# Optimization experiments

Measured on AMD Instinct MI355X. Metric: run time of the kernel, lower is better.

## Reference

```python
import jax, jax.numpy as jnp
import numpy as np
from jax import lax

B, N, M, K, C_IN = 4, 8192, 2048, 64, 64
RADIUS = 0.2
OUT_DIMS = [64, 64, 128]
BN_EPS = 1e-5


def _fps(pts):
    # pts: (N,3) -> (M,) int32 furthest-point-sampling indices, seeded at index 0
    n = pts.shape[0]
    def step(carry, _):
        mind, last = carry
        d = jnp.sum((pts - pts[last]) ** 2, axis=-1)   # dist^2 to newest centroid
        mind = jnp.minimum(mind, d)                    # dist^2 to selected set
        nxt = jnp.argmax(mind).astype(jnp.int32)
        return (mind, nxt), nxt
    init = (jnp.full((n,), 1e10, pts.dtype), jnp.int32(0))
    _, rest = lax.scan(step, init, None, length=M - 1)
    return jnp.concatenate([jnp.zeros((1,), jnp.int32), rest])


def _ball_query(qp, sp):
    # qp: (M,3) centroids, sp: (N,3) -> (M,K) first K in-radius indices, padded with first hit
    d2 = jnp.sum((qp[:, None, :] - sp[None, :, :]) ** 2, axis=-1)  # (M,N)
    score = jnp.where(d2 < RADIUS ** 2, jnp.arange(N, dtype=jnp.int32), jnp.int32(N))
    idx = -lax.top_k(-score, K)[0]          # K smallest scores = first K in-radius indices
    valid = idx < N
    first = jnp.where(valid[:, :1], idx[:, :1], 0)  # pointnet2 pads with first neighbor (or 0)
    return jnp.where(valid, idx, first)


def _forward(s_points, s_feats, Ws, gs, bs):
    pts = jnp.transpose(s_points, (0, 2, 1))    # (B,N,3)
    feats = jnp.transpose(s_feats, (0, 2, 1))   # (B,N,C)
    fps_idx = jax.vmap(_fps)(pts)               # (B,M)
    q = jnp.take_along_axis(pts, fps_idx[:, :, None], axis=1)      # (B,M,3)
    nbr_idx = jax.vmap(_ball_query)(q, pts)     # (B,M,K)
    nbr_pts = jax.vmap(lambda p, i: p[i])(pts, nbr_idx)            # (B,M,K,3)
    nbr_fts = jax.vmap(lambda f, i: f[i])(feats, nbr_idx)          # (B,M,K,C)
    # mini-PointNet input: [relative coords, neighbor feats] -> (B,M,K,3+C)
    x = jnp.concatenate([nbr_pts - q[:, :, None, :], nbr_fts], axis=-1)
    for W, g, b in zip(Ws, gs, bs):
        x = jnp.einsum('bmkc,oc->bmko', x, W)   # shared 1x1 conv
        mu = jnp.mean(x, axis=(0, 1, 2), keepdims=True)             # BatchNorm (train-mode stats)
        var = jnp.mean((x - mu) ** 2, axis=(0, 1, 2), keepdims=True)
        x = jax.nn.relu((x - mu) * lax.rsqrt(var + BN_EPS) * g + b)
    q_feats = jnp.transpose(jnp.max(x, axis=2), (0, 2, 1))          # max-pool over K -> (B,C_out,M)
    return jnp.transpose(q, (0, 2, 1)), q_feats


def setup_inputs() -> dict:
    key = jax.random.key(0)
    ks = jax.random.split(key, 8)
    inp = {
        's_points': jax.random.uniform(ks[0], (B, 3, N), jnp.float32),
        's_feats': jax.random.normal(ks[1], (B, C_IN, N), jnp.float32),
    }
    dims = [C_IN + 3] + OUT_DIMS
    for i in range(3):
        inp[f'W{i}'] = jax.random.normal(ks[2 + i], (dims[i + 1], dims[i]), jnp.float32) / np.float32(np.sqrt(dims[i]))
        inp[f'g{i}'] = jnp.ones((dims[i + 1],), jnp.float32)
        inp[f'b{i}'] = jnp.zeros((dims[i + 1],), jnp.float32)
    return inp


def reference(s_points, s_feats, W0, g0, b0, W1, g1, b1, W2, g2, b2):
    return _forward(s_points, s_feats, (W0, W1, W2), (g0, g1, g2), (b0, b1, b2))
```

## Files before the change

kernel.cpp:

```cpp
#include <hip/hip_runtime.h>
#include <math.h>


constexpr int B = 4, N = 8192, M = 2048, K = 64;
constexpr int C0 = 67;
constexpr int NB_CHAIN = B * M;
constexpr int NROW = B * M * K;

#define DEVFN static __device__ __forceinline__

template <int CTRL>
DEVFN float dpp_shift0(float x) {
  return __uint_as_float((unsigned)__builtin_amdgcn_update_dpp(
      0, (int)__float_as_uint(x), CTRL, 0xf, 0xf, true));
}

__global__ __launch_bounds__(256) void transpose_kernel(
    const float* __restrict__ P, const float* __restrict__ F,
    float4* __restrict__ pts4, float* __restrict__ ft)
{
  int g = blockIdx.x * 256 + threadIdx.x;
  int b = g >> 13, i = g & (N - 1);
  const float* Pb = P + (size_t)b * 3 * N;
  pts4[g] = make_float4(Pb[i], Pb[N + i], Pb[2 * N + i], 0.f);
  const float* Fb = F + (size_t)b * 64 * N;
  float* o = ft + (size_t)g * 64;
  #pragma unroll 8
  for (int c = 0; c < 64; ++c) o[c] = Fb[(size_t)c * N + i];
}

__global__ __launch_bounds__(256) void prep_weights(
    const float* __restrict__ W0, const float* __restrict__ W1,
    const float* __restrict__ W2,
    float* __restrict__ w0T, float* __restrict__ w1T, float* __restrict__ w2T)
{
  int t = threadIdx.x;
  for (int x = t; x < 67 * 64; x += 256) { int k = x >> 6, o = x & 63;  w0T[x] = W0[o * 67 + k]; }
  for (int x = t; x < 64 * 64; x += 256) { int k = x >> 6, o = x & 63;  w1T[x] = W1[o * 64 + k]; }
  for (int x = t; x < 64 * 128; x += 256){ int k = x >> 7, o = x & 127; w2T[x] = W2[o * 64 + k]; }
}

constexpr int FPS_T = 512;
constexpr int FPS_PT = N / FPS_T;

__global__ __launch_bounds__(512) void fps_kernel(
    const float* __restrict__ P, float4* __restrict__ q4, float* __restrict__ out_q)
{
  __shared__ float4 sp4[N];
  __shared__ __align__(16) unsigned long long partial[2][8];
  __shared__ unsigned short swidx[M];
  const int b = blockIdx.x, tid = threadIdx.x;
  const float* Pb = P + (size_t)b * 3 * N;

  float px[FPS_PT], py[FPS_PT], pz[FPS_PT], mind[FPS_PT];
  #pragma unroll
  for (int j = 0; j < FPS_PT; ++j) {
    int i = tid * FPS_PT + j;
    px[j] = Pb[i]; py[j] = Pb[N + i]; pz[j] = Pb[2 * N + i];
    sp4[i] = make_float4(px[j], py[j], pz[j], 0.f);
    mind[j] = 1e10f;
  }
  if (tid == 0) swidx[0] = 0;
  __syncthreads();

  float cx = Pb[0], cy = Pb[N], cz = Pb[2 * N];

  for (int s = 1; s < M; ++s) {
    float bv = -1.f; int bi = 0;
    #pragma unroll
    for (int j = 0; j < FPS_PT; ++j) {
      float dx = __fsub_rn(px[j], cx), dy = __fsub_rn(py[j], cy), dz = __fsub_rn(pz[j], cz);
      float d  = __fadd_rn(__fadd_rn(__fmul_rn(dx, dx), __fmul_rn(dy, dy)), __fmul_rn(dz, dz));
      float mm = fminf(mind[j], d);
      mind[j] = mm;
      bool tk = mm > bv;
      bv = tk ? mm : bv;
      bi = tk ? tid * FPS_PT + j : bi;
    }
    float r = bv;
    r = fmaxf(r, dpp_shift0<0x111>(r));
    r = fmaxf(r, dpp_shift0<0x112>(r));
    r = fmaxf(r, dpp_shift0<0x114>(r));
    r = fmaxf(r, dpp_shift0<0x118>(r));
    r = fmaxf(r, dpp_shift0<0x142>(r));
    r = fmaxf(r, dpp_shift0<0x143>(r));
    float wv = __shfl(r, 63);
    unsigned long long tied = __ballot(bv == wv);
    int wl = __ffsll(tied) - 1;
    int wi = __shfl(bi, wl);
    unsigned long long key =
        ((unsigned long long)__float_as_uint(wv) << 32) | (unsigned int)(~wi);
    const int buf = s & 1;
    if ((tid & 63) == 0) partial[buf][tid >> 6] = key;
    __syncthreads();
    unsigned long long k0 = partial[buf][0];
    #pragma unroll
    for (int w = 1; w < 8; ++w) {
      unsigned long long o = partial[buf][w];
      k0 = (o > k0) ? o : k0;
    }
    const int widx = (int)(~(unsigned int)(k0 & 0xFFFFFFFFull));
    const float4 c = sp4[widx];
    cx = c.x; cy = c.y; cz = c.z;
    if (tid == 0) swidx[s] = (unsigned short)widx;
  }
  __syncthreads();
  for (int s = tid; s < M; s += FPS_T) {
    const float4 c = sp4[swidx[s]];
    q4[b * M + s] = c;
    out_q[b * 3 * M + s]         = c.x;
    out_q[b * 3 * M + M + s]     = c.y;
    out_q[b * 3 * M + 2 * M + s] = c.z;
  }
}

__global__ __launch_bounds__(256) void ballquery_kernel(
    const float4* __restrict__ pts4, const float4* __restrict__ q4, int* __restrict__ nbr)
{
  __shared__ int slot[4][K];
  const int wv = threadIdx.x >> 6, lane = threadIdx.x & 63;
  const int qid = blockIdx.x * 4 + wv;
  const int b = qid >> 11;
  const float4 qc = q4[qid];
  const float4* pb = pts4 + (size_t)b * N;
  const float r2 = 0.04f;
  int count = 0;
  for (int c0 = 0; c0 < N; c0 += 64) {
    float4 p = pb[c0 + lane];
    float dx = __fsub_rn(p.x, qc.x), dy = __fsub_rn(p.y, qc.y), dz = __fsub_rn(p.z, qc.z);
    float d2 = __fadd_rn(__fadd_rn(__fmul_rn(dx, dx), __fmul_rn(dy, dy)), __fmul_rn(dz, dz));
    bool in = d2 < r2;
    unsigned long long mask = __ballot(in);
    int pos = count + (int)__popcll(mask & ((1ull << lane) - 1ull));
    if (in && pos < K) slot[wv][pos] = c0 + lane;
    count += (int)__popcll(mask);
    if (count >= K) break;
  }
  __syncthreads();
  int valid = count < K ? count : K;
  int v = 0;
  if (valid > 0) {
    int first = slot[wv][0];
    v = (lane < valid) ? slot[wv][lane] : first;
  }
  nbr[(size_t)qid * K + lane] = v;
}

DEVFN void conv_tile(float acc[8][8], const float (&xt)[C0 + 1][64],
                     const float* __restrict__ wT, int KK, int OC, int choff, int rg)
{
  #pragma unroll
  for (int i = 0; i < 8; ++i)
    #pragma unroll
    for (int j = 0; j < 8; ++j) acc[i][j] = 0.f;
  for (int k = 0; k < KK; ++k) {
    const float4 xa = *(const float4*)&xt[k][rg * 8];
    const float4 xb = *(const float4*)&xt[k][rg * 8 + 4];
    const float4 wa = *(const float4*)(wT + (size_t)k * OC + choff);
    const float4 wb = *(const float4*)(wT + (size_t)k * OC + choff + 4);
    const float xs[8] = {xa.x, xa.y, xa.z, xa.w, xb.x, xb.y, xb.z, xb.w};
    const float wv[8] = {wa.x, wa.y, wa.z, wa.w, wb.x, wb.y, wb.z, wb.w};
    #pragma unroll
    for (int i = 0; i < 8; ++i)
      #pragma unroll
      for (int j = 0; j < 8; ++j) acc[i][j] = fmaf(xs[i], wv[j], acc[i][j]);
  }
}

DEVFN void bn_relu_store(const float acc[8][8], const float* __restrict__ sc,
                         const float* __restrict__ sh, int choff, int rg,
                         float (&xt)[C0 + 1][64])
{
  float4 s0 = *(const float4*)(sc + choff), s1 = *(const float4*)(sc + choff + 4);
  float4 h0 = *(const float4*)(sh + choff), h1 = *(const float4*)(sh + choff + 4);
  const float scv[8] = {s0.x, s0.y, s0.z, s0.w, s1.x, s1.y, s1.z, s1.w};
  const float shv[8] = {h0.x, h0.y, h0.z, h0.w, h1.x, h1.y, h1.z, h1.w};
  __syncthreads();
  #pragma unroll
  for (int j = 0; j < 8; ++j) {
    float4 a, b;
    a.x = fmaxf(fmaf(acc[0][j], scv[j], shv[j]), 0.f);
    a.y = fmaxf(fmaf(acc[1][j], scv[j], shv[j]), 0.f);
    a.z = fmaxf(fmaf(acc[2][j], scv[j], shv[j]), 0.f);
    a.w = fmaxf(fmaf(acc[3][j], scv[j], shv[j]), 0.f);
    b.x = fmaxf(fmaf(acc[4][j], scv[j], shv[j]), 0.f);
    b.y = fmaxf(fmaf(acc[5][j], scv[j], shv[j]), 0.f);
    b.z = fmaxf(fmaf(acc[6][j], scv[j], shv[j]), 0.f);
    b.w = fmaxf(fmaf(acc[7][j], scv[j], shv[j]), 0.f);
    *(float4*)&xt[choff + j][rg * 8]     = a;
    *(float4*)&xt[choff + j][rg * 8 + 4] = b;
  }
  __syncthreads();
}

DEVFN void stats_tile(const float acc[8][8], int chbase, int lane, int qid,
                      float* __restrict__ Psum, float* __restrict__ Psq)
{
  #pragma unroll
  for (int j = 0; j < 8; ++j) {
    float s = 0.f, q = 0.f;
    #pragma unroll
    for (int i = 0; i < 8; ++i) { s += acc[i][j]; q = fmaf(acc[i][j], acc[i][j], q); }
    s += __shfl_xor(s, 8);  q += __shfl_xor(q, 8);
    s += __shfl_xor(s, 16); q += __shfl_xor(q, 16);
    s += __shfl_xor(s, 32); q += __shfl_xor(q, 32);
    if ((lane >> 3) == 0) {
      Psum[(size_t)(chbase + j) * NB_CHAIN + qid] = s;
      Psq [(size_t)(chbase + j) * NB_CHAIN + qid] = q;
    }
  }
}

DEVFN void maxmin_tile(const float acc[8][8], int chbase, int lane, int qid,
                       float* __restrict__ ymax, float* __restrict__ ymin)
{
  #pragma unroll
  for (int j = 0; j < 8; ++j) {
    float mx = acc[0][j], mn = acc[0][j];
    #pragma unroll
    for (int i = 1; i < 8; ++i) { mx = fmaxf(mx, acc[i][j]); mn = fminf(mn, acc[i][j]); }
    mx = fmaxf(mx, __shfl_xor(mx, 8));  mn = fminf(mn, __shfl_xor(mn, 8));
    mx = fmaxf(mx, __shfl_xor(mx, 16)); mn = fminf(mn, __shfl_xor(mn, 16));
    mx = fmaxf(mx, __shfl_xor(mx, 32)); mn = fminf(mn, __shfl_xor(mn, 32));
    if ((lane >> 3) == 0) {
      ymax[(size_t)(chbase + j) * NB_CHAIN + qid] = mx;
      ymin[(size_t)(chbase + j) * NB_CHAIN + qid] = mn;
    }
  }
}

DEVFN void gather_x0(const float4* __restrict__ pts4, const float* __restrict__ ft,
                     const float4* __restrict__ q4, const int* __restrict__ nbr,
                     int qid, int b, int lane, float (&xt)[C0 + 1][64])
{
  const int i = nbr[(size_t)qid * K + lane];
  const float4 qc = q4[qid];
  const float4 p = pts4[(size_t)b * N + i];
  xt[0][lane] = p.x - qc.x;
  xt[1][lane] = p.y - qc.y;
  xt[2][lane] = p.z - qc.z;
  const float4* fr = (const float4*)(ft + (size_t)(b * N + i) * 64);
  #pragma unroll
  for (int c = 0; c < 16; ++c) {
    float4 f = fr[c];
    xt[3 + 4 * c + 0][lane] = f.x;
    xt[3 + 4 * c + 1][lane] = f.y;
    xt[3 + 4 * c + 2][lane] = f.z;
    xt[3 + 4 * c + 3][lane] = f.w;
  }
  __syncthreads();
}

DEVFN void y_store(const float acc[8][8], float* __restrict__ y, int qid, int rg, int cg)
{
  float* base = y + (size_t)qid * 4096 + (size_t)(cg * 8) * 64 + rg * 8;
  #pragma unroll
  for (int j = 0; j < 8; ++j) {
    float4 a = make_float4(acc[0][j], acc[1][j], acc[2][j], acc[3][j]);
    float4 c = make_float4(acc[4][j], acc[5][j], acc[6][j], acc[7][j]);
    *(float4*)(base + (size_t)j * 64)     = a;
    *(float4*)(base + (size_t)j * 64 + 4) = c;
  }
}
DEVFN void y_load(float acc[8][8], const float* __restrict__ y, int qid, int rg, int cg)
{
  const float* base = y + (size_t)qid * 4096 + (size_t)(cg * 8) * 64 + rg * 8;
  #pragma unroll
  for (int j = 0; j < 8; ++j) {
    float4 a = *(const float4*)(base + (size_t)j * 64);
    float4 c = *(const float4*)(base + (size_t)j * 64 + 4);
    acc[0][j] = a.x; acc[1][j] = a.y; acc[2][j] = a.z; acc[3][j] = a.w;
    acc[4][j] = c.x; acc[5][j] = c.y; acc[6][j] = c.z; acc[7][j] = c.w;
  }
}

__global__ __launch_bounds__(64) void chain_p1(
    const float4* __restrict__ pts4, const float* __restrict__ ft,
    const float4* __restrict__ q4, const int* __restrict__ nbr,
    const float* __restrict__ w0T,
    float* __restrict__ Psum, float* __restrict__ Psq, float* __restrict__ y)
{
  __shared__ float xt[C0 + 1][64];
  const int qid = blockIdx.x, b = qid >> 11, lane = threadIdx.x;
  const int rg = lane >> 3, cg = lane & 7;
  gather_x0(pts4, ft, q4, nbr, qid, b, lane, xt);
  float acc[8][8];
  conv_tile(acc, xt, w0T, 67, 64, cg * 8, rg);
  stats_tile(acc, cg * 8, lane, qid, Psum, Psq);
  y_store(acc, y, qid, rg, cg);
}

template <int LAYER>
__global__ __launch_bounds__(64) void chain_p23(
    const float* __restrict__ wT, const float* __restrict__ sc,
    const float* __restrict__ sh,
    float* __restrict__ Psum, float* __restrict__ Psq,
    float* __restrict__ y, float* __restrict__ ymax, float* __restrict__ ymin)
{
  __shared__ float xt[C0 + 1][64];
  const int qid = blockIdx.x, lane = threadIdx.x;
  const int rg = lane >> 3, cg = lane & 7;
  float acc[8][8];
  y_load(acc, y, qid, rg, cg);
  bn_relu_store(acc, sc, sh, cg * 8, rg, xt);
  if (LAYER == 2) {
    conv_tile(acc, xt, wT, 64, 64, cg * 8, rg);
    stats_tile(acc, cg * 8, lane, qid, Psum, Psq);
    y_store(acc, y, qid, rg, cg);
  } else {
    conv_tile(acc, xt, wT, 64, 128, cg * 8, rg);
    stats_tile(acc, cg * 8, lane, qid, Psum, Psq);
    maxmin_tile(acc, cg * 8, lane, qid, ymax, ymin);
    conv_tile(acc, xt, wT, 64, 128, 64 + cg * 8, rg);
    stats_tile(acc, 64 + cg * 8, lane, qid, Psum, Psq);
    maxmin_tile(acc, 64 + cg * 8, lane, qid, ymax, ymin);
  }
}

template <int PHASE>
__global__ __launch_bounds__(64) void chain_kernel(
    const float4* __restrict__ pts4, const float* __restrict__ ft,
    const float4* __restrict__ q4, const int* __restrict__ nbr,
    const float* __restrict__ w0T, const float* __restrict__ w1T, const float* __restrict__ w2T,
    const float* __restrict__ sc1, const float* __restrict__ sh1,
    const float* __restrict__ sc2, const float* __restrict__ sh2,
    float* __restrict__ Psum, float* __restrict__ Psq,
    float* __restrict__ ymax, float* __restrict__ ymin)
{
  __shared__ float xt[C0 + 1][64];
  const int qid = blockIdx.x, b = qid >> 11, lane = threadIdx.x;
  const int rg = lane >> 3, cg = lane & 7;
  gather_x0(pts4, ft, q4, nbr, qid, b, lane, xt);
  float acc[8][8];
  conv_tile(acc, xt, w0T, 67, 64, cg * 8, rg);
  if (PHASE == 1) { stats_tile(acc, cg * 8, lane, qid, Psum, Psq); return; }
  bn_relu_store(acc, sc1, sh1, cg * 8, rg, xt);
  conv_tile(acc, xt, w1T, 64, 64, cg * 8, rg);
  if (PHASE == 2) { stats_tile(acc, cg * 8, lane, qid, Psum, Psq); return; }
  bn_relu_store(acc, sc2, sh2, cg * 8, rg, xt);
  conv_tile(acc, xt, w2T, 64, 128, cg * 8, rg);
  stats_tile(acc, cg * 8, lane, qid, Psum, Psq);
  maxmin_tile(acc, cg * 8, lane, qid, ymax, ymin);
  conv_tile(acc, xt, w2T, 64, 128, 64 + cg * 8, rg);
  stats_tile(acc, 64 + cg * 8, lane, qid, Psum, Psq);
  maxmin_tile(acc, 64 + cg * 8, lane, qid, ymax, ymin);
}

__global__ __launch_bounds__(256) void reduce_stats(
    const float* __restrict__ Psum, const float* __restrict__ Psq,
    const float* __restrict__ g, const float* __restrict__ beta,
    float* __restrict__ scale, float* __restrict__ shift)
{
  __shared__ float ls[256], lq[256];
  const int o = blockIdx.x, t = threadIdx.x;
  float s = 0.f, q = 0.f;
  for (int x = t; x < NB_CHAIN; x += 256) {
    s += Psum[(size_t)o * NB_CHAIN + x];
    q += Psq [(size_t)o * NB_CHAIN + x];
  }
  ls[t] = s; lq[t] = q;
  __syncthreads();
  for (int st = 128; st > 0; st >>= 1) {
    if (t < st) { ls[t] += ls[t + st]; lq[t] += lq[t + st]; }
    __syncthreads();
  }
  if (t == 0) {
    const float inv = 1.f / (float)NROW;
    float mu = ls[0] * inv;
    float var = lq[0] * inv - mu * mu;
    float scv = g[o] / sqrtf(var + 1e-5f);
    scale[o] = scv;
    shift[o] = beta[o] - mu * scv;
  }
}

__global__ __launch_bounds__(256) void bn_final(
    const float* __restrict__ ymax, const float* __restrict__ ymin,
    const float* __restrict__ sc3, const float* __restrict__ sh3,
    float* __restrict__ out1)
{
  const int idx = blockIdx.x * 256 + threadIdx.x;
  const int ch = (idx >> 11) & 127;
  const int qid = ((idx >> 18) << 11) | (idx & 2047);
  const float sc = sc3[ch], sh = sh3[ch];
  const float v = (sc >= 0.f) ? ymax[(size_t)ch * NB_CHAIN + qid]
                              : ymin[(size_t)ch * NB_CHAIN + qid];
  out1[idx] = fmaxf(fmaf(v, sc, sh), 0.f);
}

extern "C" void kernel_launch(void* const* d_in, const int* in_sizes, int n_in,
                              void* d_out, int out_size, void* d_ws, size_t ws_size,
                              hipStream_t stream)
{
  const float* P  = (const float*)d_in[0];
  const float* F  = (const float*)d_in[1];
  const float* W0 = (const float*)d_in[2];
  const float* g0 = (const float*)d_in[3];
  const float* b0 = (const float*)d_in[4];
  const float* W1 = (const float*)d_in[5];
  const float* g1 = (const float*)d_in[6];
  const float* b1 = (const float*)d_in[7];
  const float* W2 = (const float*)d_in[8];
  const float* g2 = (const float*)d_in[9];
  const float* b2 = (const float*)d_in[10];

  float* out_q = (float*)d_out;
  float* out_f = out_q + B * 3 * M;

  char* w = (char*)d_ws;
  size_t off = 0;
  auto alloc = [&](size_t bytes) -> void* {
    off = (off + 255) & ~(size_t)255;
    void* p = w + off;
    off += bytes;
    return p;
  };
  float4* pts4 = (float4*)alloc((size_t)B * N * sizeof(float4));
  float*  ft   = (float*) alloc((size_t)B * N * 64 * 4);
  float*  w0T  = (float*) alloc(68 * 64 * 4);
  float*  w1T  = (float*) alloc(64 * 64 * 4);
  float*  w2T  = (float*) alloc(64 * 128 * 4);
  float4* q4   = (float4*)alloc((size_t)B * M * sizeof(float4));
  int*    nbr  = (int*)   alloc((size_t)B * M * K * 4);
  float*  Psum = (float*) alloc((size_t)128 * NB_CHAIN * 4);
  float*  Psq  = (float*) alloc((size_t)128 * NB_CHAIN * 4);
  float*  ymax = (float*) alloc((size_t)128 * NB_CHAIN * 4);
  float*  ymin = (float*) alloc((size_t)128 * NB_CHAIN * 4);
  float*  bnp  = (float*) alloc(6 * 128 * 4);
  float *sc1 = bnp, *sh1 = bnp + 128, *sc2 = bnp + 256, *sh2 = bnp + 384,
        *sc3 = bnp + 512, *sh3 = bnp + 640;
  const size_t ybytes = (size_t)NB_CHAIN * 64 * 64 * 4;
  off = (off + 255) & ~(size_t)255;
  const bool have_y = (off + ybytes) <= ws_size;
  float* y = (float*)(w + off);
  (void)in_sizes; (void)n_in; (void)out_size;

  transpose_kernel<<<B * N / 256, 256, 0, stream>>>(P, F, pts4, ft);
  prep_weights<<<1, 256, 0, stream>>>(W0, W1, W2, w0T, w1T, w2T);
  fps_kernel<<<B, FPS_T, 0, stream>>>(P, q4, out_q);
  ballquery_kernel<<<B * M / 4, 256, 0, stream>>>(pts4, q4, nbr);

  if (have_y) {
    chain_p1<<<NB_CHAIN, 64, 0, stream>>>(pts4, ft, q4, nbr, w0T, Psum, Psq, y);
    reduce_stats<<<64, 256, 0, stream>>>(Psum, Psq, g0, b0, sc1, sh1);
    chain_p23<2><<<NB_CHAIN, 64, 0, stream>>>(w1T, sc1, sh1, Psum, Psq, y, ymax, ymin);
    reduce_stats<<<64, 256, 0, stream>>>(Psum, Psq, g1, b1, sc2, sh2);
    chain_p23<3><<<NB_CHAIN, 64, 0, stream>>>(w2T, sc2, sh2, Psum, Psq, y, ymax, ymin);
    reduce_stats<<<128, 256, 0, stream>>>(Psum, Psq, g2, b2, sc3, sh3);
  } else {
    chain_kernel<1><<<NB_CHAIN, 64, 0, stream>>>(pts4, ft, q4, nbr, w0T, w1T, w2T,
        sc1, sh1, sc2, sh2, Psum, Psq, ymax, ymin);
    reduce_stats<<<64, 256, 0, stream>>>(Psum, Psq, g0, b0, sc1, sh1);
    chain_kernel<2><<<NB_CHAIN, 64, 0, stream>>>(pts4, ft, q4, nbr, w0T, w1T, w2T,
        sc1, sh1, sc2, sh2, Psum, Psq, ymax, ymin);
    reduce_stats<<<64, 256, 0, stream>>>(Psum, Psq, g1, b1, sc2, sh2);
    chain_kernel<3><<<NB_CHAIN, 64, 0, stream>>>(pts4, ft, q4, nbr, w0T, w1T, w2T,
        sc1, sh1, sc2, sh2, Psum, Psq, ymax, ymin);
    reduce_stats<<<128, 256, 0, stream>>>(Psum, Psq, g2, b2, sc3, sh3);
  }
  bn_final<<<NB_CHAIN * 128 / 256, 256, 0, stream>>>(ymax, ymin, sc3, sh3, out_f);
}
```

Before: 2.346 ms.

## Prune FPS work with spatial cell bounding boxes and per-cell max keys

Rewrites furthest-point sampling to bin points into 128 spatial cells sorted in shared memory, each with a bounding box and a cached best (mindist, index) key. Each iteration updates only the cells whose bounding box lies closer to the new centroid than their current max min-distance, then reduces the 128 cell keys. This avoids touching all 8192 points every step. In exchange it adds extra syncs per iteration, lower parallelism when few cells are active, and more complex tie-breaking logic.

```diff
diff --git a/kernel.cpp b/kernel.cpp
--- a/kernel.cpp
+++ b/kernel.cpp
@@ -13,6 +13,29 @@
 DEVFN float dpp_shift0(float x) {
   return __uint_as_float((unsigned)__builtin_amdgcn_update_dpp(
       0, (int)__float_as_uint(x), CTRL, 0xf, 0xf, true));
+}
+template <int CTRL>
+DEVFN unsigned dpp_shift0u(unsigned x) {
+  return (unsigned)__builtin_amdgcn_update_dpp(0, (int)x, CTRL, 0xf, 0xf, true);
+}
+DEVFN float wave_max_f32(float x) {
+  x = fmaxf(x, dpp_shift0<0x111>(x));
+  x = fmaxf(x, dpp_shift0<0x112>(x));
+  x = fmaxf(x, dpp_shift0<0x114>(x));
+  x = fmaxf(x, dpp_shift0<0x118>(x));
+  x = fmaxf(x, dpp_shift0<0x142>(x));
+  x = fmaxf(x, dpp_shift0<0x143>(x));
+  return __shfl(x, 63);
+}
+DEVFN unsigned wave_max_u32(unsigned x) {
+  unsigned t;
+  t = dpp_shift0u<0x111>(x); x = x > t ? x : t;
+  t = dpp_shift0u<0x112>(x); x = x > t ? x : t;
+  t = dpp_shift0u<0x114>(x); x = x > t ? x : t;
+  t = dpp_shift0u<0x118>(x); x = x > t ? x : t;
+  t = dpp_shift0u<0x142>(x); x = x > t ? x : t;
+  t = dpp_shift0u<0x143>(x); x = x > t ? x : t;
+  return (unsigned)__shfl((int)x, 63);
 }
 
 __global__ __launch_bounds__(256) void transpose_kernel(
@@ -41,76 +64,154 @@
 }
 
 constexpr int FPS_T = 512;
-constexpr int FPS_PT = N / FPS_T;
 
 __global__ __launch_bounds__(512) void fps_kernel(
     const float* __restrict__ P, float4* __restrict__ q4, float* __restrict__ out_q)
 {
-  __shared__ float4 sp4[N];
-  __shared__ __align__(16) unsigned long long partial[2][8];
+  __shared__ float sx[N], sy[N], sz[N];
+  __shared__ float smind[N];
+  __shared__ unsigned short ssidx[N];
+  __shared__ float bb[6][128];
+  __shared__ unsigned long long bkey[128];
+  __shared__ unsigned short bspos[128];
+  __shared__ int starts[129];
+  __shared__ int hist[128];
+  __shared__ unsigned short act[2][64];
+  __shared__ int nact[2];
   __shared__ unsigned short swidx[M];
+  __shared__ float cc[3];
+  __shared__ int spos0;
+
   const int b = blockIdx.x, tid = threadIdx.x;
+  const int wv = tid >> 6, lane = tid & 63;
   const float* Pb = P + (size_t)b * 3 * N;
 
-  float px[FPS_PT], py[FPS_PT], pz[FPS_PT], mind[FPS_PT];
-  #pragma unroll
-  for (int j = 0; j < FPS_PT; ++j) {
-    int i = tid * FPS_PT + j;
-    px[j] = Pb[i]; py[j] = Pb[N + i]; pz[j] = Pb[2 * N + i];
-    sp4[i] = make_float4(px[j], py[j], pz[j], 0.f);
-    mind[j] = 1e10f;
-  }
-  if (tid == 0) swidx[0] = 0;
-  __syncthreads();
-
-  float cx = Pb[0], cy = Pb[N], cz = Pb[2 * N];
+  float lx[16], ly[16], lz[16]; int lcid[16];
+  if (tid < 128) hist[tid] = 0;
+  __syncthreads();
+  #pragma unroll
+  for (int j = 0; j < 16; ++j) {
+    int i = tid + j * FPS_T;
+    lx[j] = Pb[i]; ly[j] = Pb[N + i]; lz[j] = Pb[2 * N + i];
+    int cxi = min((int)(lx[j] * 4.f), 3);
+    int cyi = min((int)(ly[j] * 4.f), 3);
+    int czi = min((int)(lz[j] * 8.f), 7);
+    lcid[j] = (cxi << 5) | (cyi << 3) | czi;
+    atomicAdd(&hist[lcid[j]], 1);
+  }
+  __syncthreads();
+  if (tid == 0) {
+    int acc = 0;
+    for (int k = 0; k < 128; ++k) { starts[k] = acc; acc += hist[k]; }
+    starts[128] = acc;
+  }
+  __syncthreads();
+  if (tid < 128) hist[tid] = starts[tid];
+  __syncthreads();
+  #pragma unroll
+  for (int j = 0; j < 16; ++j) {
+    int i = tid + j * FPS_T;
+    int pos = atomicAdd(&hist[lcid[j]], 1);
+    sx[pos] = lx[j]; sy[pos] = ly[j]; sz[pos] = lz[j];
+    ssidx[pos] = (unsigned short)i;
+    smind[pos] = 1e10f;
+    if (i == 0) spos0 = pos;
+  }
+  __syncthreads();
+  if (tid < 128) {
+    int s0 = starts[tid], s1 = starts[tid + 1];
+    float xlo = 1e30f, xhi = -1e30f, ylo = 1e30f, yhi = -1e30f, zlo = 1e30f, zhi = -1e30f;
+    unsigned mor = 0; unsigned short msp = 0;
+    for (int p = s0; p < s1; ++p) {
+      float x = sx[p], y = sy[p], z = sz[p];
+      xlo = fminf(xlo, x); xhi = fmaxf(xhi, x);
+      ylo = fminf(ylo, y); yhi = fmaxf(yhi, y);
+      zlo = fminf(zlo, z); zhi = fmaxf(zhi, z);
+      unsigned no = ~(unsigned)ssidx[p];
+      if (no > mor) { mor = no; msp = (unsigned short)p; }
+    }
+    bb[0][tid] = xlo; bb[1][tid] = xhi; bb[2][tid] = ylo;
+    bb[3][tid] = yhi; bb[4][tid] = zlo; bb[5][tid] = zhi;
+    bkey[tid] = (s1 > s0)
+        ? (((unsigned long long)__float_as_uint(1e10f) << 32) | mor) : 0ull;
+    bspos[tid] = msp;
+  }
+  if (tid == 0) swidx[0] = (unsigned short)spos0;
+  __syncthreads();
+  float cx = sx[spos0], cy = sy[spos0], cz = sz[spos0];
 
   for (int s = 1; s < M; ++s) {
-    float bv = -1.f; int bi = 0;
-    #pragma unroll
-    for (int j = 0; j < FPS_PT; ++j) {
-      float dx = __fsub_rn(px[j], cx), dy = __fsub_rn(py[j], cy), dz = __fsub_rn(pz[j], cz);
-      float d  = __fadd_rn(__fadd_rn(__fmul_rn(dx, dx), __fmul_rn(dy, dy)), __fmul_rn(dz, dz));
-      float mm = fminf(mind[j], d);
-      mind[j] = mm;
-      bool tk = mm > bv;
-      bv = tk ? mm : bv;
-      bi = tk ? tid * FPS_PT + j : bi;
+    if (tid < 128) {
+      float ax = fmaxf(0.f, fmaxf(__fsub_rn(bb[0][tid], cx), __fsub_rn(cx, bb[1][tid])));
+      float ay = fmaxf(0.f, fmaxf(__fsub_rn(bb[2][tid], cy), __fsub_rn(cy, bb[3][tid])));
+      float az = fmaxf(0.f, fmaxf(__fsub_rn(bb[4][tid], cz), __fsub_rn(cz, bb[5][tid])));
+      float dlow = __fadd_rn(__fadd_rn(__fmul_rn(ax, ax), __fmul_rn(ay, ay)), __fmul_rn(az, az));
+      float ub = __uint_as_float((unsigned)(bkey[tid] >> 32));
+      bool actv = dlow < ub;
+      unsigned long long am = __ballot(actv);
+      int pos = (int)__popcll(am & ((1ull << lane) - 1ull));
+      if (actv) act[wv][pos] = (unsigned short)tid;
+      if (lane == 0) nact[wv] = (int)__popcll(am);
     }
-    float r = bv;
-    r = fmaxf(r, dpp_shift0<0x111>(r));
-    r = fmaxf(r, dpp_shift0<0x112>(r));
-    r = fmaxf(r, dpp_shift0<0x114>(r));
-    r = fmaxf(r, dpp_shift0<0x118>(r));
-    r = fmaxf(r, dpp_shift0<0x142>(r));
-    r = fmaxf(r, dpp_shift0<0x143>(r));
-    float wv = __shfl(r, 63);
-    unsigned long long tied = __ballot(bv == wv);
-    int wl = __ffsll(tied) - 1;
-    int wi = __shfl(bi, wl);
-    unsigned long long key =
-        ((unsigned long long)__float_as_uint(wv) << 32) | (unsigned int)(~wi);
-    const int buf = s & 1;
-    if ((tid & 63) == 0) partial[buf][tid >> 6] = key;
     __syncthreads();
-    unsigned long long k0 = partial[buf][0];
-    #pragma unroll
-    for (int w = 1; w < 8; ++w) {
-      unsigned long long o = partial[buf][w];
-      k0 = (o > k0) ? o : k0;
+    const int n0 = nact[0], ntot = n0 + nact[1];
+    for (int a = wv; a < ntot; a += 8) {
+      int k = (a < n0) ? act[0][a] : act[1][a - n0];
+      int s0 = starts[k], s1 = starts[k + 1];
+      unsigned long long bestk = 0ull, myrec = 0ull;
+      int cp = 0;
+      for (int off = s0; off < s1; off += 64) {
+        int p = off + lane;
+        float nm = -1.f; unsigned mor = 0u;
+        if (p < s1) {
+          float dx = __fsub_rn(sx[p], cx), dy = __fsub_rn(sy[p], cy), dz = __fsub_rn(sz[p], cz);
+          float d = __fadd_rn(__fadd_rn(__fmul_rn(dx, dx), __fmul_rn(dy, dy)), __fmul_rn(dz, dz));
+          nm = fminf(smind[p], d);
+          smind[p] = nm;
+          mor = ~(unsigned)ssidx[p];
+        }
+        float wvmax = wave_max_f32(nm);
+        unsigned cand = (nm == wvmax) ? mor : 0u;
+        unsigned wor = wave_max_u32(cand);
+        unsigned long long kk =
+            ((unsigned long long)__float_as_uint(wvmax) << 32) | wor;
+        if (nm == wvmax && mor == wor && kk > myrec) { myrec = kk; cp = p; }
+        if (kk > bestk) bestk = kk;
+      }
+      if (myrec == bestk && bestk != 0ull) {
+        bkey[k] = bestk;
+        bspos[k] = (unsigned short)cp;
+      }
     }
-    const int widx = (int)(~(unsigned int)(k0 & 0xFFFFFFFFull));
-    const float4 c = sp4[widx];
-    cx = c.x; cy = c.y; cz = c.z;
-    if (tid == 0) swidx[s] = (unsigned short)widx;
-  }
-  __syncthreads();
-  for (int s = tid; s < M; s += FPS_T) {
-    const float4 c = sp4[swidx[s]];
-    q4[b * M + s] = c;
-    out_q[b * 3 * M + s]         = c.x;
-    out_q[b * 3 * M + M + s]     = c.y;
-    out_q[b * 3 * M + 2 * M + s] = c.z;
+    __syncthreads();
+    if (wv == 0) {
+      unsigned long long k1 = bkey[lane], k2 = bkey[lane + 64];
+      unsigned long long kk = k1 > k2 ? k1 : k2;
+      float vh = __uint_as_float((unsigned)(kk >> 32));
+      float vmax = wave_max_f32(vh);
+      unsigned cand = (vh == vmax) ? (unsigned)(kk & 0xFFFFFFFFull) : 0u;
+      unsigned lomax = wave_max_u32(cand);
+      unsigned long long fin =
+          ((unsigned long long)__float_as_uint(vmax) << 32) | lomax;
+      int kwin = -1;
+      if (k1 == fin) kwin = lane;
+      if (k2 == fin) kwin = lane + 64;
+      if (kwin >= 0) {
+        int sp = bspos[kwin];
+        cc[0] = sx[sp]; cc[1] = sy[sp]; cc[2] = sz[sp];
+        swidx[s] = (unsigned short)sp;
+      }
+    }
+    __syncthreads();
+    cx = cc[0]; cy = cc[1]; cz = cc[2];
+  }
+  for (int s2 = tid; s2 < M; s2 += FPS_T) {
+    int sp = swidx[s2];
+    float xx = sx[sp], yy = sy[sp], zz = sz[sp];
+    q4[b * M + s2] = make_float4(xx, yy, zz, 0.f);
+    out_q[b * 3 * M + s2]         = xx;
+    out_q[b * 3 * M + M + s2]     = yy;
+    out_q[b * 3 * M + 2 * M + s2] = zz;
   }
 }
 
```

Result: slower. 3.417 ms (+45.6%).

## Spatially sort FPS points into voxel buckets and skip threads via bounding-box pruning

Applied to the files above, without the earlier changes.

The FPS kernel now buckets points into an 8x8x8 voxel grid with a shared-memory counting sort, so each thread holds 16 spatially clustered points and tracks their bounding box. Each iteration, a wave skips the distance update when no lane's box can come closer to the new centroid than that lane's current best min-distance, since the min-distance values cannot change in that case. Tie-breaking now carries the original index through the comparison, and the wave reduction uses DPP plus readlane in place of a shuffle and ballot. This adds sort setup and per-iteration box checks, and it only saves work when whole waves can be skipped.

```diff
diff --git a/kernel.cpp b/kernel.cpp
--- a/kernel.cpp
+++ b/kernel.cpp
@@ -13,6 +13,30 @@
 DEVFN float dpp_shift0(float x) {
   return __uint_as_float((unsigned)__builtin_amdgcn_update_dpp(
       0, (int)__float_as_uint(x), CTRL, 0xf, 0xf, true));
+}
+template <int CTRL>
+DEVFN unsigned dpp_shift0u(unsigned x) {
+  return (unsigned)__builtin_amdgcn_update_dpp(0, (int)x, CTRL, 0xf, 0xf, true);
+}
+DEVFN float wave_max_bcast_f(float x) {
+  x = fmaxf(x, dpp_shift0<0x111>(x));
+  x = fmaxf(x, dpp_shift0<0x112>(x));
+  x = fmaxf(x, dpp_shift0<0x114>(x));
+  x = fmaxf(x, dpp_shift0<0x118>(x));
+  x = fmaxf(x, dpp_shift0<0x142>(x));
+  x = fmaxf(x, dpp_shift0<0x143>(x));
+  return __uint_as_float(
+      (unsigned)__builtin_amdgcn_readlane((int)__float_as_uint(x), 63));
+}
+DEVFN unsigned wave_max_bcast_u(unsigned x) {
+  unsigned t;
+  t = dpp_shift0u<0x111>(x); x = x > t ? x : t;
+  t = dpp_shift0u<0x112>(x); x = x > t ? x : t;
+  t = dpp_shift0u<0x114>(x); x = x > t ? x : t;
+  t = dpp_shift0u<0x118>(x); x = x > t ? x : t;
+  t = dpp_shift0u<0x142>(x); x = x > t ? x : t;
+  t = dpp_shift0u<0x143>(x); x = x > t ? x : t;
+  return (unsigned)__builtin_amdgcn_readlane((int)x, 63);
 }
 
 __global__ __launch_bounds__(256) void transpose_kernel(
@@ -41,57 +65,99 @@
 }
 
 constexpr int FPS_T = 512;
-constexpr int FPS_PT = N / FPS_T;
+constexpr int FPS_PT = 16;
 
 __global__ __launch_bounds__(512) void fps_kernel(
     const float* __restrict__ P, float4* __restrict__ q4, float* __restrict__ out_q)
 {
   __shared__ float4 sp4[N];
+  __shared__ unsigned short ssort[N];
+  __shared__ int hist[512];
   __shared__ __align__(16) unsigned long long partial[2][8];
   __shared__ unsigned short swidx[M];
+
   const int b = blockIdx.x, tid = threadIdx.x;
+  const int wvid = tid >> 6, lane = tid & 63;
   const float* Pb = P + (size_t)b * 3 * N;
 
+  hist[tid & 511] = 0;
+  __syncthreads();
+
+  int lcid[FPS_PT];
+  #pragma unroll
+  for (int j = 0; j < FPS_PT; ++j) {
+    int i = tid + j * FPS_T;
+    float x = Pb[i], y = Pb[N + i], z = Pb[2 * N + i];
+    sp4[i] = make_float4(x, y, z, 0.f);
+    int cxi = min((int)(x * 8.f), 7);
+    int cyi = min((int)(y * 8.f), 7);
+    int czi = min((int)(z * 8.f), 7);
+    lcid[j] = (cxi << 6) | (cyi << 3) | czi;
+    atomicAdd(&hist[lcid[j]], 1);
+  }
+  __syncthreads();
+  if (tid == 0) {
+    int acc = 0;
+    for (int k = 0; k < 512; ++k) { int t = hist[k]; hist[k] = acc; acc += t; }
+  }
+  __syncthreads();
+  #pragma unroll
+  for (int j = 0; j < FPS_PT; ++j) {
+    int i = tid + j * FPS_T;
+    int pos = atomicAdd(&hist[lcid[j]], 1);
+    ssort[pos] = (unsigned short)i;
+  }
+  __syncthreads();
+
   float px[FPS_PT], py[FPS_PT], pz[FPS_PT], mind[FPS_PT];
+  unsigned noid[FPS_PT];
+  float xlo = 1e30f, xhi = -1e30f, ylo = 1e30f, yhi = -1e30f, zlo = 1e30f, zhi = -1e30f;
+  unsigned bno = 0;
   #pragma unroll
   for (int j = 0; j < FPS_PT; ++j) {
-    int i = tid * FPS_PT + j;
-    px[j] = Pb[i]; py[j] = Pb[N + i]; pz[j] = Pb[2 * N + i];
-    sp4[i] = make_float4(px[j], py[j], pz[j], 0.f);
+    int o = ssort[tid * FPS_PT + j];
+    float4 p = sp4[o];
+    px[j] = p.x; py[j] = p.y; pz[j] = p.z;
+    noid[j] = ~(unsigned)o;
     mind[j] = 1e10f;
-  }
+    xlo = fminf(xlo, p.x); xhi = fmaxf(xhi, p.x);
+    ylo = fminf(ylo, p.y); yhi = fmaxf(yhi, p.y);
+    zlo = fminf(zlo, p.z); zhi = fmaxf(zhi, p.z);
+    bno = noid[j] > bno ? noid[j] : bno;
+  }
+  float bv = 1e10f;
   if (tid == 0) swidx[0] = 0;
-  __syncthreads();
-
-  float cx = Pb[0], cy = Pb[N], cz = Pb[2 * N];
+  float4 c0 = sp4[0];
+  float cx = c0.x, cy = c0.y, cz = c0.z;
 
   for (int s = 1; s < M; ++s) {
-    float bv = -1.f; int bi = 0;
-    #pragma unroll
-    for (int j = 0; j < FPS_PT; ++j) {
-      float dx = __fsub_rn(px[j], cx), dy = __fsub_rn(py[j], cy), dz = __fsub_rn(pz[j], cz);
-      float d  = __fadd_rn(__fadd_rn(__fmul_rn(dx, dx), __fmul_rn(dy, dy)), __fmul_rn(dz, dz));
-      float mm = fminf(mind[j], d);
-      mind[j] = mm;
-      bool tk = mm > bv;
-      bv = tk ? mm : bv;
-      bi = tk ? tid * FPS_PT + j : bi;
+    float ax = fmaxf(0.f, fmaxf(__fsub_rn(xlo, cx), __fsub_rn(cx, xhi)));
+    float ay = fmaxf(0.f, fmaxf(__fsub_rn(ylo, cy), __fsub_rn(cy, yhi)));
+    float az = fmaxf(0.f, fmaxf(__fsub_rn(zlo, cz), __fsub_rn(cz, zhi)));
+    float dlow = __fadd_rn(__fadd_rn(__fmul_rn(ax, ax), __fmul_rn(ay, ay)), __fmul_rn(az, az));
+    bool active = dlow < bv;
+    if (__ballot(active) != 0ull) {
+      float nbv = -1.f; unsigned nbn = 0u;
+      #pragma unroll
+      for (int j = 0; j < FPS_PT; ++j) {
+        float dx = __fsub_rn(px[j], cx), dy = __fsub_rn(py[j], cy), dz = __fsub_rn(pz[j], cz);
+        float d  = __fadd_rn(__fadd_rn(__fmul_rn(dx, dx), __fmul_rn(dy, dy)), __fmul_rn(dz, dz));
+        float mm = fminf(mind[j], d);
+        mind[j] = mm;
+        bool t1 = mm > nbv;
+        bool t2 = (mm == nbv) & (noid[j] > nbn);
+        bool tk = t1 | t2;
+        nbv = tk ? mm : nbv;
+        nbn = tk ? noid[j] : nbn;
+      }
+      bv = nbv; bno = nbn;
     }
-    float r = bv;
-    r = fmaxf(r, dpp_shift0<0x111>(r));
-    r = fmaxf(r, dpp_shift0<0x112>(r));
-    r = fmaxf(r, dpp_shift0<0x114>(r));
-    r = fmaxf(r, dpp_shift0<0x118>(r));
-    r = fmaxf(r, dpp_shift0<0x142>(r));
-    r = fmaxf(r, dpp_shift0<0x143>(r));
-    float wv = __shfl(r, 63);
-    unsigned long long tied = __ballot(bv == wv);
-    int wl = __ffsll(tied) - 1;
-    int wi = __shfl(bi, wl);
-    unsigned long long key =
-        ((unsigned long long)__float_as_uint(wv) << 32) | (unsigned int)(~wi);
+    float vmax = wave_max_bcast_f(bv);
+    unsigned cand = (bv == vmax) ? bno : 0u;
+    unsigned wor = wave_max_bcast_u(cand);
     const int buf = s & 1;
-    if ((tid & 63) == 0) partial[buf][tid >> 6] = key;
+    if (lane == 0)
+      partial[buf][wvid] = ((unsigned long long)__float_as_uint(vmax) << 32) | wor;
     __syncthreads();
     unsigned long long k0 = partial[buf][0];
     #pragma unroll
@@ -99,18 +165,18 @@
       unsigned long long o = partial[buf][w];
       k0 = (o > k0) ? o : k0;
     }
-    const int widx = (int)(~(unsigned int)(k0 & 0xFFFFFFFFull));
-    const float4 c = sp4[widx];
+    const int worig = (int)((~(unsigned)(k0 & 0xFFFFFFFFull)) & (unsigned)(N - 1));
+    const float4 c = sp4[worig];
     cx = c.x; cy = c.y; cz = c.z;
-    if (tid == 0) swidx[s] = (unsigned short)widx;
-  }
-  __syncthreads();
-  for (int s = tid; s < M; s += FPS_T) {
-    const float4 c = sp4[swidx[s]];
-    q4[b * M + s] = c;
-    out_q[b * 3 * M + s]         = c.x;
-    out_q[b * 3 * M + M + s]     = c.y;
-    out_q[b * 3 * M + 2 * M + s] = c.z;
+    if (tid == 0) swidx[s] = (unsigned short)worig;
+  }
+  __syncthreads();
+  for (int s2 = tid; s2 < M; s2 += FPS_T) {
+    const float4 c = sp4[swidx[s2]];
+    q4[b * M + s2] = c;
+    out_q[b * 3 * M + s2]         = c.x;
+    out_q[b * 3 * M + M + s2]     = c.y;
+    out_q[b * 3 * M + 2 * M + s2] = c.z;
   }
 }
 
```

Measured after the change: 2.615 ms. +11.5%, slower.
